# Kernel optimization log

Hardware: AMD Instinct MI355X
Metric: run time of the kernel (lower is better)

The kernel has to match this reference:

```python
import jax, jax.numpy as jnp
import numpy as np

# FineMatching constants (from init_kwargs)
GRID_NUM = 8
VOXEL = 0.04
NDIM = 3
MAX_NEIGHBORS = 128
OFFSET = GRID_NUM * VOXEL / 2.0           # 0.16
RADIUS = (GRID_NUM + 1) * VOXEL / 2.0      # 0.18
G1 = GRID_NUM + 1                          # grid nodes per dim
G = G1 ** NDIM                             # 729 flattened voxel bins
NEG_BIG = -1e30


def setup_inputs() -> dict:
    key = jax.random.key(0)
    k1, k2, k3, k4, k5 = jax.random.split(key, 5)
    B, L0, L1, C = 4, 2048, 2048, 64
    x0 = jax.random.normal(k1, (B, L0, C), dtype=jnp.float32)
    x1 = jax.random.normal(k2, (B, L1, C), dtype=jnp.float32)
    pos0 = jax.random.uniform(k3, (B, L0, 3), dtype=jnp.float32)
    pos1 = jax.random.uniform(k4, (B, L1, 3), dtype=jnp.float32)
    pad_mask = jax.random.uniform(k5, (B, L1)) < 0.1  # True = padded / masked out
    return {"x0": x0, "x1": x1, "pos0": pos0, "pos1": pos1, "pad_mask": pad_mask}


def reference(x0, x1, pos0, pos1, pad_mask):
    B, L0, C = x0.shape
    K = MAX_NEIGHBORS
    # --- radius neighbor search (per batch, dense distances, K nearest) ---
    d2 = jnp.sum((pos0[:, :, None, :] - pos1[:, None, :, :]) ** 2, axis=-1)  # (B,L0,L1)
    neg_d2, idx = jax.lax.top_k(-d2, K)                                       # (B,L0,K)
    valid = (-neg_d2) < RADIUS ** 2                                           # within radius
    pad_g = jnp.take_along_axis(pad_mask[:, None, :], idx, axis=2)           # (B,L0,K)
    valid = valid & (~pad_g)
    # --- edge-wise gather + correlation ---
    x1g = jnp.take_along_axis(x1[:, None, :, :], idx[..., None], axis=2)     # (B,L0,K,C)
    corr = jnp.einsum('blc,blkc->blk', x0, x1g) / jnp.sqrt(jnp.float32(C))
    # --- masked segment softmax over neighbors (nan -> 0 when no valid edge) ---
    logits = jnp.where(valid, corr, NEG_BIG)
    prob = jax.nn.softmax(logits, axis=-1) * valid                            # (B,L0,K)
    # --- flow aggregation ---
    pos1g = jnp.take_along_axis(pos1[:, None, :, :], idx[..., None], axis=2) # (B,L0,K,3)
    dpos = pos1g - pos0[:, :, None, :]
    flow = jnp.einsum('blk,blkd->bld', prob, dpos)                            # (B,L0,3)
    # --- P2G voxel scatter: bin prob mass into (grid_num+1)^3 voxel grid ---
    coords = (dpos + OFFSET) / VOXEL
    vox = jnp.clip(jnp.round(coords), 0, GRID_NUM).astype(jnp.int32)          # (B,L0,K,3)
    flat = (vox[..., 0] * G1 + vox[..., 1]) * G1 + vox[..., 2]                # (B,L0,K)
    b_ix = jnp.arange(B)[:, None, None]
    l_ix = jnp.arange(L0)[None, :, None]
    flow_dist = jnp.zeros((B, L0, G), dtype=x0.dtype).at[b_ix, l_ix, flat].add(prob)
    return flow, flow_dist
```

## Files before the change

kernel.cpp:

```cpp
#include <hip/hip_runtime.h>
#include <stdint.h>

#define NB    4
#define NL0   2048
#define NL1   2048
#define NC    64
#define KMAX  128
#define CAP   256
#define NG1   9
#define NBINS 729
#define FLOWN (NB*NL0*3)
#define QPB   8
#define TPB   512

__global__ __launch_bounds__(TPB, 6) void fine_match_kernel(
    const float* __restrict__ x0, const float* __restrict__ x1,
    const float* __restrict__ pos0, const float* __restrict__ pos1,
    const void* __restrict__ padraw, float* __restrict__ out)
{
  __shared__ float          s_pos[3][NL1];
  __shared__ uint8_t        s_pad[NL1];
  __shared__ float          s_x0[QPB][NC];
  __shared__ float          s_p0[QPB][3];
  __shared__ unsigned short s_jj[QPB][CAP];
  __shared__ float          s_flow[QPB][3];
  __shared__ int            s_a01, s_af;

  const int t = threadIdx.x;
  const int bid = blockIdx.x;
  const int b = bid >> 8;
  const int l0base = (bid & 255) * QPB;

  if (t == 0) { s_a01 = 1; s_af = 1; }
  __syncthreads();

  {
    const uint32_t* pi = (const uint32_t*)padraw;
    bool a01 = true, af = true;
    for (int i = t; i < (NB*NL1)/4; i += TPB) {
      const uint32_t v = pi[i];
      a01 = a01 && (v == 0u || v == 1u);
      af  = af  && (v == 0u || v == 0x3F800000u);
    }
    if (!a01) atomicAnd(&s_a01, 0);
    if (!af)  atomicAnd(&s_af, 0);
  }

  {
    const float* p1b = pos1 + b*NL1*3;
    for (int i = t; i < NL1*3; i += TPB) {
      const float v = p1b[i];
      const int j = i / 3, c = i - j*3;
      s_pos[c][j] = v;
    }
  }
  {
    const int q = t >> 6, c = t & 63;
    s_x0[q][c] = x0[(b*NL0 + l0base + q)*NC + c];
  }
  if (t < QPB*3) {
    const int q = t / 3, c = t - q*3;
    s_p0[q][c] = pos0[(b*NL0 + l0base + q)*3 + c];
  }
  {
    float4 z4; z4.x = z4.y = z4.z = z4.w = 0.0f;
    float4* bz = (float4*)(out + FLOWN + (size_t)(b*NL0 + l0base)*NBINS);
    for (int i = t; i < QPB*NBINS/4; i += TPB) bz[i] = z4;
  }
  __syncthreads();

  {
    const int mode = s_a01 ? 1 : (s_af ? 2 : 0);
    if (mode == 1) {
      const int32_t* p = (const int32_t*)padraw + b*NL1;
      for (int i = t; i < NL1; i += TPB) s_pad[i] = (p[i] != 0);
    } else if (mode == 2) {
      const float* p = (const float*)padraw + b*NL1;
      for (int i = t; i < NL1; i += TPB) s_pad[i] = (p[i] != 0.0f);
    } else {
      const uint8_t* p = (const uint8_t*)padraw + b*NL1;
      for (int i = t; i < NL1; i += TPB) s_pad[i] = p[i];
    }
  }
  __syncthreads();

  const int wv = t >> 6, lane = t & 63;
  const int l0 = l0base + wv;
  const float p0x = s_p0[wv][0], p0y = s_p0[wv][1], p0z = s_p0[wv][2];

  int cnt = 0;
  for (int base = 0; base < NL1; base += 64) {
    const int j = base + lane;
    const float dx = __fsub_rn(s_pos[0][j], p0x);
    const float dy = __fsub_rn(s_pos[1][j], p0y);
    const float dz = __fsub_rn(s_pos[2][j], p0z);
    const float d2 = __fadd_rn(__fadd_rn(__fmul_rn(dx,dx), __fmul_rn(dy,dy)), __fmul_rn(dz,dz));
    const bool ok = d2 < 0.0324f;
    const uint64_t m = __ballot(ok);
    if (ok) {
      const int pos = cnt + (int)__popcll(m & ((1ull << lane) - 1ull));
      if (pos < CAP) s_jj[wv][pos] = (unsigned short)j;
    }
    cnt += (int)__popcll(m);
  }
  if (cnt > CAP) cnt = CAP;
  __syncthreads();

  const bool over = (cnt > KMAX);
  float corr[4]; bool keep[4];
  #pragma unroll
  for (int s = 0; s < 4; ++s) {
    keep[s] = false; corr[s] = -1e30f;
    const int i = lane + 64*s;
    if (i < cnt) {
      const int j = (int)s_jj[wv][i];
      bool k = (s_pad[j] == 0);
      if (over && k) {
        const float dx = __fsub_rn(s_pos[0][j], p0x);
        const float dy = __fsub_rn(s_pos[1][j], p0y);
        const float dz = __fsub_rn(s_pos[2][j], p0z);
        const float di = __fadd_rn(__fadd_rn(__fmul_rn(dx,dx), __fmul_rn(dy,dy)), __fmul_rn(dz,dz));
        int rank = 0;
        for (int m2 = 0; m2 < cnt; ++m2) {
          const int jm = (int)s_jj[wv][m2];
          const float ex = __fsub_rn(s_pos[0][jm], p0x);
          const float ey = __fsub_rn(s_pos[1][jm], p0y);
          const float ez = __fsub_rn(s_pos[2][jm], p0z);
          const float dm = __fadd_rn(__fadd_rn(__fmul_rn(ex,ex), __fmul_rn(ey,ey)), __fmul_rn(ez,ez));
          rank += (dm < di || (dm == di && m2 < i)) ? 1 : 0;
        }
        if (rank >= KMAX) k = false;
      }
      if (k) {
        const float* xr = x1 + (b*NL1 + j)*NC;
        float acc = 0.0f;
        #pragma unroll
        for (int c = 0; c < NC; c += 4) {
          const float4 v = *(const float4*)(xr + c);
          acc += s_x0[wv][c+0]*v.x + s_x0[wv][c+1]*v.y
               + s_x0[wv][c+2]*v.z + s_x0[wv][c+3]*v.w;
        }
        corr[s] = acc * 0.125f;
        keep[s] = true;
      }
    }
  }

  float mx = -1e30f;
  #pragma unroll
  for (int s = 0; s < 4; ++s) if (keep[s] && corr[s] > mx) mx = corr[s];
  for (int off = 32; off; off >>= 1) { const float o = __shfl_xor(mx, off); if (o > mx) mx = o; }
  float pr[4]; float sum = 0.0f;
  #pragma unroll
  for (int s = 0; s < 4; ++s) { pr[s] = keep[s] ? expf(corr[s] - mx) : 0.0f; sum += pr[s]; }
  for (int off = 32; off; off >>= 1) sum += __shfl_xor(sum, off);
  const float inv = (sum > 0.0f) ? (1.0f / sum) : 0.0f;

  float* bins = out + FLOWN + (size_t)(b*NL0 + l0)*NBINS;
  float fx = 0.0f, fy = 0.0f, fz = 0.0f;
  #pragma unroll
  for (int s = 0; s < 4; ++s) {
    if (!keep[s]) continue;
    const float pv = pr[s] * inv;
    const int j = (int)s_jj[wv][lane + 64*s];
    const float dx = __fsub_rn(s_pos[0][j], p0x);
    const float dy = __fsub_rn(s_pos[1][j], p0y);
    const float dz = __fsub_rn(s_pos[2][j], p0z);
    fx += pv*dx; fy += pv*dy; fz += pv*dz;
    const float cx = __fdiv_rn(__fadd_rn(dx, 0.16f), 0.04f);
    const float cy = __fdiv_rn(__fadd_rn(dy, 0.16f), 0.04f);
    const float cz = __fdiv_rn(__fadd_rn(dz, 0.16f), 0.04f);
    int vx = (int)rintf(cx); vx = vx < 0 ? 0 : (vx > 8 ? 8 : vx);
    int vy = (int)rintf(cy); vy = vy < 0 ? 0 : (vy > 8 ? 8 : vy);
    int vz = (int)rintf(cz); vz = vz < 0 ? 0 : (vz > 8 ? 8 : vz);
    __hip_atomic_fetch_add(&bins[(vx*NG1 + vy)*NG1 + vz], pv,
                           __ATOMIC_RELAXED, __HIP_MEMORY_SCOPE_WORKGROUP);
  }
  for (int off = 32; off; off >>= 1) {
    fx += __shfl_xor(fx, off); fy += __shfl_xor(fy, off); fz += __shfl_xor(fz, off);
  }
  if (lane == 0) { s_flow[wv][0] = fx; s_flow[wv][1] = fy; s_flow[wv][2] = fz; }
  __syncthreads();

  if (t < QPB*3) {
    float* f = out + (size_t)(b*NL0 + l0base)*3;
    f[t] = (&s_flow[0][0])[t];
  }
}

extern "C" void kernel_launch(void* const* d_in, const int* in_sizes, int n_in,
                              void* d_out, int out_size, void* d_ws, size_t ws_size,
                              hipStream_t stream) {
  const float* x0   = (const float*)d_in[0];
  const float* x1   = (const float*)d_in[1];
  const float* pos0 = (const float*)d_in[2];
  const float* pos1 = (const float*)d_in[3];
  const void*  pad  = d_in[4];
  float* out = (float*)d_out;
  (void)in_sizes; (void)n_in; (void)out_size; (void)d_ws; (void)ws_size;
  hipLaunchKernelGGL(fine_match_kernel, dim3(NB*NL0/QPB), dim3(TPB), 0, stream,
                     x0, x1, pos0, pos1, pad, out);
}
```

Measured before the change: 32.36 us.

## Hoist pad-format detection and pos1 transposition into separate prep kernels

Pad-mask format detection, which every block used to redo over the whole mask, moves into a tiny detect kernel. A prep kernel then converts the mask to uint8 and transposes pos1 into a structure-of-arrays workspace, so the main kernel can load both with vectorized copies. The main kernel also doubles queries per block to 16 with 1024 threads, reads x0 from shared memory as float4, adds early loop exits based on the neighbor count, and writes flow directly from lane 0 instead of staging it through shared memory. The cost is extra kernel launches plus a memset, and a larger block size that may lower occupancy.

Measured after the change: 39.74 us. +22.8%, slower.

```diff
diff --git a/kernel.cpp b/kernel.cpp
--- a/kernel.cpp
+++ b/kernel.cpp
@@ -10,56 +10,76 @@
 #define NG1   9
 #define NBINS 729
 #define FLOWN (NB*NL0*3)
-#define QPB   8
-#define TPB   512
-
-__global__ __launch_bounds__(TPB, 6) void fine_match_kernel(
+#define QPB   16
+#define TPB   1024
+
+#define WS_PAD   64
+#define WS_POS   8256
+
+__global__ __launch_bounds__(256) void detect_kernel(
+    const uint32_t* __restrict__ pad, uint32_t* __restrict__ flags)
+{
+  const int i = blockIdx.x*256 + threadIdx.x;
+  const uint32_t v = pad[i];
+  int a01 = (v <= 1u);
+  int af  = (v == 0u || v == 0x3F800000u);
+  a01 = __syncthreads_and(a01);
+  af  = __syncthreads_and(af);
+  if (threadIdx.x == 0) {
+    if (!a01) atomicAnd(&flags[0], 0u);
+    if (!af)  atomicAnd(&flags[1], 0u);
+  }
+}
+
+__global__ __launch_bounds__(256) void prep_kernel(
+    const void* __restrict__ padraw, const float* __restrict__ pos1,
+    const uint32_t* __restrict__ flags, uint8_t* __restrict__ padu8,
+    float* __restrict__ possoa)
+{
+  const int g = blockIdx.x*256 + threadIdx.x;
+  const int mode = flags[0] ? 1 : (flags[1] ? 2 : 0);
+  uint8_t pv;
+  if (mode == 1)      pv = (((const int32_t*)padraw)[g] != 0);
+  else if (mode == 2) pv = (((const float*)padraw)[g] != 0.0f);
+  else                pv = ((const uint8_t*)padraw)[g];
+  padu8[g] = pv;
+  #pragma unroll
+  for (int k = 0; k < 3; ++k) {
+    const int i = g + k*8192;
+    const float v = pos1[i];
+    const int b = i / 6144;
+    const int r = i - b*6144;
+    const int j = r / 3;
+    const int c = r - j*3;
+    possoa[(b*3 + c)*NL1 + j] = v;
+  }
+}
+
+__global__ __launch_bounds__(TPB, 8) void fine_match_kernel(
     const float* __restrict__ x0, const float* __restrict__ x1,
-    const float* __restrict__ pos0, const float* __restrict__ pos1,
-    const void* __restrict__ padraw, float* __restrict__ out)
+    const float* __restrict__ pos0, const float* __restrict__ possoa,
+    const uint8_t* __restrict__ padu8, float* __restrict__ out)
 {
   __shared__ float          s_pos[3][NL1];
   __shared__ uint8_t        s_pad[NL1];
-  __shared__ float          s_x0[QPB][NC];
+  __shared__ float          s_x0[QPB*NC];
   __shared__ float          s_p0[QPB][3];
   __shared__ unsigned short s_jj[QPB][CAP];
-  __shared__ float          s_flow[QPB][3];
-  __shared__ int            s_a01, s_af;
 
   const int t = threadIdx.x;
   const int bid = blockIdx.x;
-  const int b = bid >> 8;
-  const int l0base = (bid & 255) * QPB;
-
-  if (t == 0) { s_a01 = 1; s_af = 1; }
-  __syncthreads();
+  const int b = bid >> 7;
+  const int l0base = (bid & 127) * QPB;
 
   {
-    const uint32_t* pi = (const uint32_t*)padraw;
-    bool a01 = true, af = true;
-    for (int i = t; i < (NB*NL1)/4; i += TPB) {
-      const uint32_t v = pi[i];
-      a01 = a01 && (v == 0u || v == 1u);
-      af  = af  && (v == 0u || v == 0x3F800000u);
-    }
-    if (!a01) atomicAnd(&s_a01, 0);
-    if (!af)  atomicAnd(&s_af, 0);
-  }
-
-  {
-    const float* p1b = pos1 + b*NL1*3;
-    for (int i = t; i < NL1*3; i += TPB) {
-      const float v = p1b[i];
-      const int j = i / 3, c = i - j*3;
-      s_pos[c][j] = v;
-    }
-  }
-  {
-    const int q = t >> 6, c = t & 63;
-    s_x0[q][c] = x0[(b*NL0 + l0base + q)*NC + c];
-  }
+    const float4* src = (const float4*)(possoa + (size_t)b*3*NL1);
+    float4* dst = (float4*)(&s_pos[0][0]);
+    for (int i = t; i < 3*NL1/4; i += TPB) dst[i] = src[i];
+  }
+  if (t < NL1/4) ((uint32_t*)s_pad)[t] = ((const uint32_t*)(padu8 + b*NL1))[t];
+  s_x0[t] = x0[(size_t)(b*NL0 + l0base)*NC + t];
   if (t < QPB*3) {
-    const int q = t / 3, c = t - q*3;
+    const int q = t/3, c = t - q*3;
     s_p0[q][c] = pos0[(b*NL0 + l0base + q)*3 + c];
   }
   {
@@ -69,26 +89,12 @@
   }
   __syncthreads();
 
-  {
-    const int mode = s_a01 ? 1 : (s_af ? 2 : 0);
-    if (mode == 1) {
-      const int32_t* p = (const int32_t*)padraw + b*NL1;
-      for (int i = t; i < NL1; i += TPB) s_pad[i] = (p[i] != 0);
-    } else if (mode == 2) {
-      const float* p = (const float*)padraw + b*NL1;
-      for (int i = t; i < NL1; i += TPB) s_pad[i] = (p[i] != 0.0f);
-    } else {
-      const uint8_t* p = (const uint8_t*)padraw + b*NL1;
-      for (int i = t; i < NL1; i += TPB) s_pad[i] = p[i];
-    }
-  }
-  __syncthreads();
-
   const int wv = t >> 6, lane = t & 63;
   const int l0 = l0base + wv;
   const float p0x = s_p0[wv][0], p0y = s_p0[wv][1], p0z = s_p0[wv][2];
 
   int cnt = 0;
+  #pragma unroll 4
   for (int base = 0; base < NL1; base += 64) {
     const int j = base + lane;
     const float dx = __fsub_rn(s_pos[0][j], p0x);
@@ -107,10 +113,11 @@
   __syncthreads();
 
   const bool over = (cnt > KMAX);
-  float corr[4]; bool keep[4];
-  #pragma unroll
+  float corr[4];
+  #pragma unroll
+  for (int s = 0; s < 4; ++s) corr[s] = -1e30f;
   for (int s = 0; s < 4; ++s) {
-    keep[s] = false; corr[s] = -1e30f;
+    if (64*s >= cnt) break;
     const int i = lane + 64*s;
     if (i < cnt) {
       const int j = (int)s_jj[wv][i];
@@ -132,35 +139,34 @@
         if (rank >= KMAX) k = false;
       }
       if (k) {
-        const float* xr = x1 + (b*NL1 + j)*NC;
+        const float* xr = x1 + ((size_t)b*NL1 + j)*NC;
         float acc = 0.0f;
         #pragma unroll
         for (int c = 0; c < NC; c += 4) {
           const float4 v = *(const float4*)(xr + c);
-          acc += s_x0[wv][c+0]*v.x + s_x0[wv][c+1]*v.y
-               + s_x0[wv][c+2]*v.z + s_x0[wv][c+3]*v.w;
+          const float4 q = *(const float4*)(&s_x0[wv*NC + c]);
+          acc += q.x*v.x + q.y*v.y + q.z*v.z + q.w*v.w;
         }
         corr[s] = acc * 0.125f;
-        keep[s] = true;
       }
     }
   }
 
   float mx = -1e30f;
   #pragma unroll
-  for (int s = 0; s < 4; ++s) if (keep[s] && corr[s] > mx) mx = corr[s];
+  for (int s = 0; s < 4; ++s) if (corr[s] > mx) mx = corr[s];
   for (int off = 32; off; off >>= 1) { const float o = __shfl_xor(mx, off); if (o > mx) mx = o; }
   float pr[4]; float sum = 0.0f;
   #pragma unroll
-  for (int s = 0; s < 4; ++s) { pr[s] = keep[s] ? expf(corr[s] - mx) : 0.0f; sum += pr[s]; }
+  for (int s = 0; s < 4; ++s) { pr[s] = (corr[s] > -1e30f) ? expf(corr[s] - mx) : 0.0f; sum += pr[s]; }
   for (int off = 32; off; off >>= 1) sum += __shfl_xor(sum, off);
   const float inv = (sum > 0.0f) ? (1.0f / sum) : 0.0f;
 
-  float* bins = out + FLOWN + (size_t)(b*NL0 + l0)*NBINS;
+  float* bins = out + FLOWN + (size_t)((size_t)b*NL0 + l0)*NBINS;
   float fx = 0.0f, fy = 0.0f, fz = 0.0f;
-  #pragma unroll
   for (int s = 0; s < 4; ++s) {
-    if (!keep[s]) continue;
+    if (64*s >= cnt) break;
+    if (pr[s] <= 0.0f) continue;
     const float pv = pr[s] * inv;
     const int j = (int)s_jj[wv][lane + 64*s];
     const float dx = __fsub_rn(s_pos[0][j], p0x);
@@ -179,12 +185,9 @@
   for (int off = 32; off; off >>= 1) {
     fx += __shfl_xor(fx, off); fy += __shfl_xor(fy, off); fz += __shfl_xor(fz, off);
   }
-  if (lane == 0) { s_flow[wv][0] = fx; s_flow[wv][1] = fy; s_flow[wv][2] = fz; }
-  __syncthreads();
-
-  if (t < QPB*3) {
-    float* f = out + (size_t)(b*NL0 + l0base)*3;
-    f[t] = (&s_flow[0][0])[t];
+  if (lane == 0) {
+    float* f = out + (size_t)((size_t)b*NL0 + l0)*3;
+    f[0] = fx; f[1] = fy; f[2] = fz;
   }
 }
 
@@ -197,7 +200,17 @@
   const float* pos1 = (const float*)d_in[3];
   const void*  pad  = d_in[4];
   float* out = (float*)d_out;
-  (void)in_sizes; (void)n_in; (void)out_size; (void)d_ws; (void)ws_size;
+  (void)in_sizes; (void)n_in; (void)out_size; (void)ws_size;
+
+  uint32_t* flags  = (uint32_t*)d_ws;
+  uint8_t*  padu8  = (uint8_t*)d_ws + WS_PAD;
+  float*    possoa = (float*)((char*)d_ws + WS_POS);
+
+  hipMemsetAsync(d_ws, 0xFF, 8, stream);
+  hipLaunchKernelGGL(detect_kernel, dim3(8), dim3(256), 0, stream,
+                     (const uint32_t*)pad, flags);
+  hipLaunchKernelGGL(prep_kernel, dim3(32), dim3(256), 0, stream,
+                     pad, pos1, flags, padu8, possoa);
   hipLaunchKernelGGL(fine_match_kernel, dim3(NB*NL0/QPB), dim3(TPB), 0, stream,
-                     x0, x1, pos0, pos1, pad, out);
-}
+                     x0, x1, pos0, possoa, padu8, out);
+}
```

## Cut shared-memory staging and syncs, read pad mask from global, raise occupancy

Applied to the files above, without the earlier changes.

Removes the separate pad-mask staging pass and its extra barriers. Pad-format detection now uses a single __syncthreads_and, and the mask is read from global memory only for candidate neighbors. pos1 is copied to shared memory as interleaved float4 instead of being transposed into SoA. Correlations are kept in shared memory rather than registers, loops exit early past the candidate count, and flow is written straight from each wave, with launch bounds raised to 8 blocks per SM. Together these aim to lower setup work, sync count and register pressure. The cost is stride-3 LDS reads, which may cause bank conflicts, plus scattered global reads of the mask.

New measurement: 29.63 us. 8.5% less time.

```diff
diff --git a/kernel.cpp b/kernel.cpp
--- a/kernel.cpp
+++ b/kernel.cpp
@@ -13,74 +13,47 @@
 #define QPB   8
 #define TPB   512
 
-__global__ __launch_bounds__(TPB, 6) void fine_match_kernel(
+__global__ __launch_bounds__(TPB, 8) void fine_match_kernel(
     const float* __restrict__ x0, const float* __restrict__ x1,
     const float* __restrict__ pos0, const float* __restrict__ pos1,
     const void* __restrict__ padraw, float* __restrict__ out)
 {
-  __shared__ float          s_pos[3][NL1];
-  __shared__ uint8_t        s_pad[NL1];
-  __shared__ float          s_x0[QPB][NC];
+  __shared__ float          s_pos[NL1*3];
+  __shared__ float          s_x0[QPB*NC];
   __shared__ float          s_p0[QPB][3];
   __shared__ unsigned short s_jj[QPB][CAP];
-  __shared__ float          s_flow[QPB][3];
-  __shared__ int            s_a01, s_af;
+  __shared__ float          s_corr[QPB][CAP];
 
   const int t = threadIdx.x;
   const int bid = blockIdx.x;
   const int b = bid >> 8;
   const int l0base = (bid & 255) * QPB;
 
-  if (t == 0) { s_a01 = 1; s_af = 1; }
-  __syncthreads();
-
+  int wide;
   {
     const uint32_t* pi = (const uint32_t*)padraw;
-    bool a01 = true, af = true;
+    int ok4 = 1;
     for (int i = t; i < (NB*NL1)/4; i += TPB) {
       const uint32_t v = pi[i];
-      a01 = a01 && (v == 0u || v == 1u);
-      af  = af  && (v == 0u || v == 0x3F800000u);
+      ok4 &= (int)((v <= 1u) | (v == 0x3F800000u));
     }
-    if (!a01) atomicAnd(&s_a01, 0);
-    if (!af)  atomicAnd(&s_af, 0);
+    wide = __syncthreads_and(ok4);
   }
 
   {
-    const float* p1b = pos1 + b*NL1*3;
-    for (int i = t; i < NL1*3; i += TPB) {
-      const float v = p1b[i];
-      const int j = i / 3, c = i - j*3;
-      s_pos[c][j] = v;
-    }
+    const float4* src = (const float4*)(pos1 + (size_t)b*NL1*3);
+    float4* dst = (float4*)s_pos;
+    for (int i = t; i < NL1*3/4; i += TPB) dst[i] = src[i];
   }
-  {
-    const int q = t >> 6, c = t & 63;
-    s_x0[q][c] = x0[(b*NL0 + l0base + q)*NC + c];
-  }
+  s_x0[t] = x0[(size_t)(b*NL0 + l0base)*NC + t];
   if (t < QPB*3) {
-    const int q = t / 3, c = t - q*3;
+    const int q = t/3, c = t - q*3;
     s_p0[q][c] = pos0[(b*NL0 + l0base + q)*3 + c];
   }
   {
     float4 z4; z4.x = z4.y = z4.z = z4.w = 0.0f;
     float4* bz = (float4*)(out + FLOWN + (size_t)(b*NL0 + l0base)*NBINS);
     for (int i = t; i < QPB*NBINS/4; i += TPB) bz[i] = z4;
-  }
-  __syncthreads();
-
-  {
-    const int mode = s_a01 ? 1 : (s_af ? 2 : 0);
-    if (mode == 1) {
-      const int32_t* p = (const int32_t*)padraw + b*NL1;
-      for (int i = t; i < NL1; i += TPB) s_pad[i] = (p[i] != 0);
-    } else if (mode == 2) {
-      const float* p = (const float*)padraw + b*NL1;
-      for (int i = t; i < NL1; i += TPB) s_pad[i] = (p[i] != 0.0f);
-    } else {
-      const uint8_t* p = (const uint8_t*)padraw + b*NL1;
-      for (int i = t; i < NL1; i += TPB) s_pad[i] = p[i];
-    }
   }
   __syncthreads();
 
@@ -91,9 +64,9 @@
   int cnt = 0;
   for (int base = 0; base < NL1; base += 64) {
     const int j = base + lane;
-    const float dx = __fsub_rn(s_pos[0][j], p0x);
-    const float dy = __fsub_rn(s_pos[1][j], p0y);
-    const float dz = __fsub_rn(s_pos[2][j], p0z);
+    const float dx = __fsub_rn(s_pos[j*3+0], p0x);
+    const float dy = __fsub_rn(s_pos[j*3+1], p0y);
+    const float dz = __fsub_rn(s_pos[j*3+2], p0z);
     const float d2 = __fadd_rn(__fadd_rn(__fmul_rn(dx,dx), __fmul_rn(dy,dy)), __fmul_rn(dz,dz));
     const bool ok = d2 < 0.0324f;
     const uint64_t m = __ballot(ok);
@@ -107,84 +80,93 @@
   __syncthreads();
 
   const bool over = (cnt > KMAX);
-  float corr[4]; bool keep[4];
-  #pragma unroll
   for (int s = 0; s < 4; ++s) {
-    keep[s] = false; corr[s] = -1e30f;
+    if (64*s >= cnt) break;
     const int i = lane + 64*s;
     if (i < cnt) {
+      float c = -1e30f;
       const int j = (int)s_jj[wv][i];
-      bool k = (s_pad[j] == 0);
+      bool k;
+      if (wide) k = (((const uint32_t*)padraw)[b*NL1 + j] == 0u);
+      else      k = (((const uint8_t*)padraw)[b*NL1 + j] == 0);
       if (over && k) {
-        const float dx = __fsub_rn(s_pos[0][j], p0x);
-        const float dy = __fsub_rn(s_pos[1][j], p0y);
-        const float dz = __fsub_rn(s_pos[2][j], p0z);
+        const float dx = __fsub_rn(s_pos[j*3+0], p0x);
+        const float dy = __fsub_rn(s_pos[j*3+1], p0y);
+        const float dz = __fsub_rn(s_pos[j*3+2], p0z);
         const float di = __fadd_rn(__fadd_rn(__fmul_rn(dx,dx), __fmul_rn(dy,dy)), __fmul_rn(dz,dz));
         int rank = 0;
         for (int m2 = 0; m2 < cnt; ++m2) {
           const int jm = (int)s_jj[wv][m2];
-          const float ex = __fsub_rn(s_pos[0][jm], p0x);
-          const float ey = __fsub_rn(s_pos[1][jm], p0y);
-          const float ez = __fsub_rn(s_pos[2][jm], p0z);
+          const float ex = __fsub_rn(s_pos[jm*3+0], p0x);
+          const float ey = __fsub_rn(s_pos[jm*3+1], p0y);
+          const float ez = __fsub_rn(s_pos[jm*3+2], p0z);
           const float dm = __fadd_rn(__fadd_rn(__fmul_rn(ex,ex), __fmul_rn(ey,ey)), __fmul_rn(ez,ez));
           rank += (dm < di || (dm == di && m2 < i)) ? 1 : 0;
         }
         if (rank >= KMAX) k = false;
       }
       if (k) {
-        const float* xr = x1 + (b*NL1 + j)*NC;
+        const float* xr = x1 + ((size_t)b*NL1 + j)*NC;
         float acc = 0.0f;
         #pragma unroll
-        for (int c = 0; c < NC; c += 4) {
-          const float4 v = *(const float4*)(xr + c);
-          acc += s_x0[wv][c+0]*v.x + s_x0[wv][c+1]*v.y
-               + s_x0[wv][c+2]*v.z + s_x0[wv][c+3]*v.w;
+        for (int cc = 0; cc < NC; cc += 4) {
+          const float4 v = *(const float4*)(xr + cc);
+          const float4 q = *(const float4*)(&s_x0[wv*NC + cc]);
+          acc += q.x*v.x + q.y*v.y + q.z*v.z + q.w*v.w;
         }
-        corr[s] = acc * 0.125f;
-        keep[s] = true;
+        c = acc * 0.125f;
       }
+      s_corr[wv][i] = c;
     }
   }
 
   float mx = -1e30f;
-  #pragma unroll
-  for (int s = 0; s < 4; ++s) if (keep[s] && corr[s] > mx) mx = corr[s];
+  for (int s = 0; s < 4; ++s) {
+    if (64*s >= cnt) break;
+    const int i = lane + 64*s;
+    if (i < cnt) { const float c = s_corr[wv][i]; if (c > mx) mx = c; }
+  }
   for (int off = 32; off; off >>= 1) { const float o = __shfl_xor(mx, off); if (o > mx) mx = o; }
-  float pr[4]; float sum = 0.0f;
-  #pragma unroll
-  for (int s = 0; s < 4; ++s) { pr[s] = keep[s] ? expf(corr[s] - mx) : 0.0f; sum += pr[s]; }
+  float sum = 0.0f;
+  for (int s = 0; s < 4; ++s) {
+    if (64*s >= cnt) break;
+    const int i = lane + 64*s;
+    if (i < cnt) { const float c = s_corr[wv][i]; if (c > -1e30f) sum += expf(c - mx); }
+  }
   for (int off = 32; off; off >>= 1) sum += __shfl_xor(sum, off);
   const float inv = (sum > 0.0f) ? (1.0f / sum) : 0.0f;
 
-  float* bins = out + FLOWN + (size_t)(b*NL0 + l0)*NBINS;
+  float* bins = out + FLOWN + (size_t)((size_t)b*NL0 + l0)*NBINS;
   float fx = 0.0f, fy = 0.0f, fz = 0.0f;
-  #pragma unroll
   for (int s = 0; s < 4; ++s) {
-    if (!keep[s]) continue;
-    const float pv = pr[s] * inv;
-    const int j = (int)s_jj[wv][lane + 64*s];
-    const float dx = __fsub_rn(s_pos[0][j], p0x);
-    const float dy = __fsub_rn(s_pos[1][j], p0y);
-    const float dz = __fsub_rn(s_pos[2][j], p0z);
-    fx += pv*dx; fy += pv*dy; fz += pv*dz;
-    const float cx = __fdiv_rn(__fadd_rn(dx, 0.16f), 0.04f);
-    const float cy = __fdiv_rn(__fadd_rn(dy, 0.16f), 0.04f);
-    const float cz = __fdiv_rn(__fadd_rn(dz, 0.16f), 0.04f);
-    int vx = (int)rintf(cx); vx = vx < 0 ? 0 : (vx > 8 ? 8 : vx);
-    int vy = (int)rintf(cy); vy = vy < 0 ? 0 : (vy > 8 ? 8 : vy);
-    int vz = (int)rintf(cz); vz = vz < 0 ? 0 : (vz > 8 ? 8 : vz);
-    __hip_atomic_fetch_add(&bins[(vx*NG1 + vy)*NG1 + vz], pv,
-                           __ATOMIC_RELAXED, __HIP_MEMORY_SCOPE_WORKGROUP);
+    if (64*s >= cnt) break;
+    const int i = lane + 64*s;
+    if (i < cnt) {
+      const float c = s_corr[wv][i];
+      if (c > -1e30f) {
+        const float pv = expf(c - mx) * inv;
+        const int j = (int)s_jj[wv][i];
+        const float dx = __fsub_rn(s_pos[j*3+0], p0x);
+        const float dy = __fsub_rn(s_pos[j*3+1], p0y);
+        const float dz = __fsub_rn(s_pos[j*3+2], p0z);
+        fx += pv*dx; fy += pv*dy; fz += pv*dz;
+        const float cx = __fdiv_rn(__fadd_rn(dx, 0.16f), 0.04f);
+        const float cy = __fdiv_rn(__fadd_rn(dy, 0.16f), 0.04f);
+        const float cz = __fdiv_rn(__fadd_rn(dz, 0.16f), 0.04f);
+        int vx = (int)rintf(cx); vx = vx < 0 ? 0 : (vx > 8 ? 8 : vx);
+        int vy = (int)rintf(cy); vy = vy < 0 ? 0 : (vy > 8 ? 8 : vy);
+        int vz = (int)rintf(cz); vz = vz < 0 ? 0 : (vz > 8 ? 8 : vz);
+        __hip_atomic_fetch_add(&bins[(vx*NG1 + vy)*NG1 + vz], pv,
+                               __ATOMIC_RELAXED, __HIP_MEMORY_SCOPE_WORKGROUP);
+      }
+    }
   }
   for (int off = 32; off; off >>= 1) {
     fx += __shfl_xor(fx, off); fy += __shfl_xor(fy, off); fz += __shfl_xor(fz, off);
   }
-  if (lane == 0) { s_flow[wv][0] = fx; s_flow[wv][1] = fy; s_flow[wv][2] = fz; }
-  __syncthreads();
-
-  if (t < QPB*3) {
-    float* f = out + (size_t)(b*NL0 + l0base)*3;
-    f[t] = (&s_flow[0][0])[t];
+  if (lane == 0) {
+    float* f = out + (size_t)((size_t)b*NL0 + l0)*3;
+    f[0] = fx; f[1] = fy; f[2] = fz;
   }
 }
 
```
